# Kernel optimization log

Hardware: AMD Instinct MI355X
Metric: run time of the kernel (lower is better)

The kernel has to match this reference:

```python
import jax, jax.numpy as jnp
import numpy as np

B, D, C = 256, 128, 8000
MARGIN = 0.5
SCALE = 64.0
EPS = 1e-12  # tf.nn.l2_normalize epsilon


def _l2_normalize(x, axis):
    # Matches tf.nn.l2_normalize: x * rsqrt(max(sum(x^2), eps))
    sq = jnp.sum(x * x, axis=axis, keepdims=True)
    return x * jax.lax.rsqrt(jnp.maximum(sq, EPS))


def setup_inputs() -> dict:
    key = jax.random.key(0)
    k1, k2, k3 = jax.random.split(key, 3)
    embds = jax.random.normal(k1, (B, D), dtype=jnp.float32)
    w = jax.random.normal(k2, (D, C), dtype=jnp.float32)
    labels = jax.random.randint(k3, (B,), 0, C, dtype=jnp.int32)
    return {"embds": embds, "w": w, "labels": labels}


def reference(embds, w, labels):
    normed_embds = _l2_normalize(embds, axis=1)          # [B, D]
    normed_w = _l2_normalize(w, axis=0)                  # [D, C]
    gr_w = normed_w.T[labels]                            # gather per-label columns -> [B, D]
    # dw[b, d, c] = gr_w[b, d] - normed_w[d, c]
    dw = gr_w[:, :, None] - normed_w[None, :, :]         # [B, D, C]
    normed_dw = _l2_normalize(dw, axis=1)                # normalize over feature dim D
    win = jnp.einsum('bd,bdc->bc', normed_embds, normed_dw)
    penalties = MARGIN - jnp.minimum(MARGIN, win)        # [B, C]
    cos_t = normed_embds @ normed_w                      # [B, C]
    logits = jax.nn.softmax(SCALE * cos_t, axis=-1)
    return (logits, penalties)
```

## Files before the change

kernel.cpp:

```cpp
#include <hip/hip_runtime.h>
#include <math.h>

#define BB 256
#define DD 128
#define CC 8000
#define EPSF 1e-12f
#define SCALEF 64.0f
#define MARGINF 0.5f

__global__ __launch_bounds__(256, 2) void fused_kernel(
    const float* __restrict__ embds, const float* __restrict__ w,
    const int* __restrict__ labels, float* __restrict__ out,
    float* __restrict__ psums) {
  __shared__ float neS[DD * 16];
  __shared__ float gS[DD * 16];
  __shared__ float s1S[16];
  __shared__ int labS[16];

  int tid = threadIdx.x;
  int c0 = blockIdx.x * 256;
  int r0 = blockIdx.y * 16;

  {
    int r = tid >> 4;
    int k = tid & 15;
    int row = r0 + r;
    int lab = labels[row];
    const float4* e4 = (const float4*)(embds + row * DD + k * 8);
    float4 ea = e4[0], eb = e4[1];
    float ev[8] = {ea.x, ea.y, ea.z, ea.w, eb.x, eb.y, eb.z, eb.w};
    float wl[8];
    float se = 0.f, sw = 0.f, sx = 0.f;
    #pragma unroll
    for (int i = 0; i < 8; ++i) {
      wl[i] = w[(k * 8 + i) * CC + lab];
      se = fmaf(ev[i], ev[i], se);
      sw = fmaf(wl[i], wl[i], sw);
      sx = fmaf(ev[i], wl[i], sx);
    }
    #pragma unroll
    for (int off = 1; off < 16; off <<= 1) {
      se += __shfl_xor(se, off, 64);
      sw += __shfl_xor(sw, off, 64);
      sx += __shfl_xor(sx, off, 64);
    }
    float rn = rsqrtf(fmaxf(se, EPSF));
    float rl = rsqrtf(fmaxf(sw, EPSF));
    #pragma unroll
    for (int i = 0; i < 8; ++i) {
      neS[(k * 8 + i) * 16 + r] = ev[i] * rn;
      gS[(k * 8 + i) * 16 + r] = wl[i] * rl;
    }
    if (k == 0) { s1S[r] = sx * rn * rl; labS[r] = lab; }
  }
  __syncthreads();

  int tx = tid & 63;
  int ty = tid >> 6;
  int c = c0 + tx * 4;
  bool cok = c < CC;
  const float4* w4 = (const float4*)w;
  int wbase = (c0 >> 2) + tx;

  float accC[4][4], accG[4][4], colsum[4];
  #pragma unroll
  for (int rr = 0; rr < 4; ++rr)
    #pragma unroll
    for (int j = 0; j < 4; ++j) { accC[rr][j] = 0.f; accG[rr][j] = 0.f; }
  #pragma unroll
  for (int j = 0; j < 4; ++j) colsum[j] = 0.f;

  #pragma unroll 8
  for (int d = 0; d < DD; ++d) {
    float4 wv = cok ? w4[d * (CC / 4) + wbase] : make_float4(0.f, 0.f, 0.f, 0.f);
    float4 a = *(const float4*)&neS[d * 16 + ty * 4];
    float4 g = *(const float4*)&gS[d * 16 + ty * 4];
    float av[4] = {a.x, a.y, a.z, a.w};
    float gv[4] = {g.x, g.y, g.z, g.w};
    float wj[4] = {wv.x, wv.y, wv.z, wv.w};
    #pragma unroll
    for (int j = 0; j < 4; ++j) colsum[j] = fmaf(wj[j], wj[j], colsum[j]);
    #pragma unroll
    for (int rr = 0; rr < 4; ++rr) {
      #pragma unroll
      for (int j = 0; j < 4; ++j) {
        accC[rr][j] = fmaf(av[rr], wj[j], accC[rr][j]);
        accG[rr][j] = fmaf(gv[rr], wj[j], accG[rr][j]);
      }
    }
  }

  float rcj[4];
  #pragma unroll
  for (int j = 0; j < 4; ++j) rcj[j] = rsqrtf(fmaxf(colsum[j], EPSF));

  float* pen_base = out + (size_t)BB * CC;
  #pragma unroll
  for (int rr = 0; rr < 4; ++rr) {
    int lr = ty * 4 + rr;
    int row = r0 + lr;
    float s1v = s1S[lr];
    int lab = labS[lr];
    float penv[4], eo[4];
    float psum = 0.f;
    #pragma unroll
    for (int j = 0; j < 4; ++j) {
      float cs = accC[rr][j] * rcj[j];
      float gw = accG[rr][j] * rcj[j];
      float win = (s1v - cs) * rsqrtf(fmaxf(2.f - 2.f * gw, EPSF));
      if (c + j == lab) win = 0.f;
      penv[j] = MARGINF - fminf(MARGINF, win);
      float e = cok ? __expf(SCALEF * cs) : 0.f;
      eo[j] = e;
      psum += e;
    }
    if (cok) {
      size_t o4 = (size_t)row * (CC / 4) + wbase;
      ((float4*)pen_base)[o4] = make_float4(penv[0], penv[1], penv[2], penv[3]);
      ((float4*)out)[o4] = make_float4(eo[0], eo[1], eo[2], eo[3]);
    }
    #pragma unroll
    for (int off = 1; off < 64; off <<= 1) psum += __shfl_xor(psum, off, 64);
    if (tx == 0) psums[row * 32 + blockIdx.x] = psum;
  }
}

__global__ __launch_bounds__(512) void scale_kernel(
    float* __restrict__ out, const float* __restrict__ psums) {
  __shared__ float invS;
  int r = blockIdx.x;
  int tid = threadIdx.x;
  if (tid < 64) {
    float p = (tid < 32) ? psums[r * 32 + tid] : 0.f;
    #pragma unroll
    for (int off = 1; off < 32; off <<= 1) p += __shfl_xor(p, off, 64);
    if (tid == 0) invS = 1.f / p;
  }
  __syncthreads();
  float inv = invS;
  float4* row = (float4*)out + (size_t)r * (CC / 4);
  #pragma unroll
  for (int k = 0; k < 4; ++k) {
    int i = tid + k * 512;
    if (i < CC / 4) {
      float4 v = row[i];
      row[i] = make_float4(v.x * inv, v.y * inv, v.z * inv, v.w * inv);
    }
  }
}

extern "C" void kernel_launch(void* const* d_in, const int* in_sizes, int n_in,
                              void* d_out, int out_size, void* d_ws, size_t ws_size,
                              hipStream_t stream) {
  const float* embds = (const float*)d_in[0];
  const float* w = (const float*)d_in[1];
  const int* labels = (const int*)d_in[2];
  float* out = (float*)d_out;
  float* psums = (float*)d_ws;

  dim3 gA(32, 16);
  fused_kernel<<<gA, 256, 0, stream>>>(embds, w, labels, out, psums);
  scale_kernel<<<256, 512, 0, stream>>>(out, psums);
}
```

Measured before the change: 93.81 us.

## Stage W tiles through double-buffered shared memory with register prefetch

Each block now loads W in 16-row tiles into a double-buffered shared-memory array. The next tile is prefetched into registers while the current one is computed, and the first tile's load overlaps the normalization prologue. Before, every thread read W float4s straight from global memory inside the d-loop. Launch bounds rise to 3 blocks per SM, and the change adds about 32KB of LDS per block plus a barrier per tile. Edge columns are clamped, so tail blocks load duplicate data rather than zeros.

```diff
diff --git a/kernel.cpp b/kernel.cpp
--- a/kernel.cpp
+++ b/kernel.cpp
@@ -8,18 +8,38 @@
 #define SCALEF 64.0f
 #define MARGINF 0.5f
 
-__global__ __launch_bounds__(256, 2) void fused_kernel(
+#define RT 16
+#define CT 256
+#define TD 16
+#define NT (DD / TD)
+
+__global__ __launch_bounds__(256, 3) void fused_kernel(
     const float* __restrict__ embds, const float* __restrict__ w,
     const int* __restrict__ labels, float* __restrict__ out,
     float* __restrict__ psums) {
-  __shared__ float neS[DD * 16];
-  __shared__ float gS[DD * 16];
-  __shared__ float s1S[16];
-  __shared__ int labS[16];
+  __shared__ float wS[2][TD][CT];
+  __shared__ float neS[DD * RT];
+  __shared__ float gS[DD * RT];
+  __shared__ float s1S[RT];
+  __shared__ int labS[RT];
 
   int tid = threadIdx.x;
-  int c0 = blockIdx.x * 256;
-  int r0 = blockIdx.y * 16;
+  int c0 = blockIdx.x * CT;
+  int r0 = blockIdx.y * RT;
+
+  int sr = tid >> 4;
+  int scb = (tid & 15) * 4;
+  int scg[4];
+  #pragma unroll
+  for (int i = 0; i < 4; ++i) {
+    int cgl = c0 + scb + i * 64;
+    scg[i] = cgl > CC - 4 ? CC - 4 : cgl;
+  }
+
+  float4 st[4];
+  #pragma unroll
+  for (int i = 0; i < 4; ++i)
+    st[i] = *(const float4*)(w + (size_t)sr * CC + scg[i]);
 
   {
     int r = tid >> 4;
@@ -53,48 +73,67 @@
     }
     if (k == 0) { s1S[r] = sx * rn * rl; labS[r] = lab; }
   }
+
+  #pragma unroll
+  for (int i = 0; i < 4; ++i) *(float4*)&wS[0][sr][scb + i * 64] = st[i];
   __syncthreads();
 
   int tx = tid & 63;
   int ty = tid >> 6;
-  int c = c0 + tx * 4;
+  int wcol = tx * 4;
+  int c = c0 + wcol;
   bool cok = c < CC;
-  const float4* w4 = (const float4*)w;
+
+  float accC[4][4], accG[4][4], colsum[4];
+  #pragma unroll
+  for (int rr = 0; rr < 4; ++rr)
+    #pragma unroll
+    for (int j = 0; j < 4; ++j) { accC[rr][j] = 0.f; accG[rr][j] = 0.f; }
+  #pragma unroll
+  for (int j = 0; j < 4; ++j) colsum[j] = 0.f;
+
+  for (int t = 0; t < NT; ++t) {
+    if (t + 1 < NT) {
+      #pragma unroll
+      for (int i = 0; i < 4; ++i)
+        st[i] = *(const float4*)(w + (size_t)((t + 1) * TD + sr) * CC + scg[i]);
+    }
+
+    const float(*wT)[CT] = wS[t & 1];
+    #pragma unroll
+    for (int dl = 0; dl < TD; ++dl) {
+      int d = t * TD + dl;
+      float4 wv = *(const float4*)&wT[dl][wcol];
+      float4 a = *(const float4*)&neS[d * 16 + ty * 4];
+      float4 g = *(const float4*)&gS[d * 16 + ty * 4];
+      float av[4] = {a.x, a.y, a.z, a.w};
+      float gv[4] = {g.x, g.y, g.z, g.w};
+      float wj[4] = {wv.x, wv.y, wv.z, wv.w};
+      #pragma unroll
+      for (int j = 0; j < 4; ++j) colsum[j] = fmaf(wj[j], wj[j], colsum[j]);
+      #pragma unroll
+      for (int rr = 0; rr < 4; ++rr)
+        #pragma unroll
+        for (int j = 0; j < 4; ++j) {
+          accC[rr][j] = fmaf(av[rr], wj[j], accC[rr][j]);
+          accG[rr][j] = fmaf(gv[rr], wj[j], accG[rr][j]);
+        }
+    }
+
+    if (t + 1 < NT) {
+      #pragma unroll
+      for (int i = 0; i < 4; ++i)
+        *(float4*)&wS[(t + 1) & 1][sr][scb + i * 64] = st[i];
+    }
+    __syncthreads();
+  }
+
+  float rcj[4];
+  #pragma unroll
+  for (int j = 0; j < 4; ++j) rcj[j] = rsqrtf(fmaxf(colsum[j], EPSF));
+
+  float* pen_base = out + (size_t)BB * CC;
   int wbase = (c0 >> 2) + tx;
-
-  float accC[4][4], accG[4][4], colsum[4];
-  #pragma unroll
-  for (int rr = 0; rr < 4; ++rr)
-    #pragma unroll
-    for (int j = 0; j < 4; ++j) { accC[rr][j] = 0.f; accG[rr][j] = 0.f; }
-  #pragma unroll
-  for (int j = 0; j < 4; ++j) colsum[j] = 0.f;
-
-  #pragma unroll 8
-  for (int d = 0; d < DD; ++d) {
-    float4 wv = cok ? w4[d * (CC / 4) + wbase] : make_float4(0.f, 0.f, 0.f, 0.f);
-    float4 a = *(const float4*)&neS[d * 16 + ty * 4];
-    float4 g = *(const float4*)&gS[d * 16 + ty * 4];
-    float av[4] = {a.x, a.y, a.z, a.w};
-    float gv[4] = {g.x, g.y, g.z, g.w};
-    float wj[4] = {wv.x, wv.y, wv.z, wv.w};
-    #pragma unroll
-    for (int j = 0; j < 4; ++j) colsum[j] = fmaf(wj[j], wj[j], colsum[j]);
-    #pragma unroll
-    for (int rr = 0; rr < 4; ++rr) {
-      #pragma unroll
-      for (int j = 0; j < 4; ++j) {
-        accC[rr][j] = fmaf(av[rr], wj[j], accC[rr][j]);
-        accG[rr][j] = fmaf(gv[rr], wj[j], accG[rr][j]);
-      }
-    }
-  }
-
-  float rcj[4];
-  #pragma unroll
-  for (int j = 0; j < 4; ++j) rcj[j] = rsqrtf(fmaxf(colsum[j], EPSF));
-
-  float* pen_base = out + (size_t)BB * CC;
   #pragma unroll
   for (int rr = 0; rr < 4; ++rr) {
     int lr = ty * 4 + rr;
```

Result: slower. 197.3 us (+110.3%).

## Fuse softmax normalization into main kernel via last-block-per-row atomic ticket

Applied to the files above, without the earlier changes.

Removes the separate scale kernel launch. Each block publishes its partial exp-sum per row and increments a per-row atomic counter. The block that arrives last for a row reduces the partial sums and rescales that whole row in place. This saves a kernel launch and its gap, but the last-arriving blocks now do serial row rescaling work. The counter is never reset and relies on modulo 32 to work across repeated calls. Visibility of the other blocks' plain stores to the exp outputs rests only on the acq_rel ticket.

```diff
diff --git a/kernel.cpp b/kernel.cpp
--- a/kernel.cpp
+++ b/kernel.cpp
@@ -8,6 +8,9 @@
 #define SCALEF 64.0f
 #define MARGINF 0.5f
 
+
+__device__ int g_tick[BB];
+
 __global__ __launch_bounds__(256, 2) void fused_kernel(
     const float* __restrict__ embds, const float* __restrict__ w,
     const int* __restrict__ labels, float* __restrict__ out,
@@ -16,10 +19,14 @@
   __shared__ float gS[DD * 16];
   __shared__ float s1S[16];
   __shared__ int labS[16];
+  __shared__ int wonS[16];
+  __shared__ float invS;
 
   int tid = threadIdx.x;
   int c0 = blockIdx.x * 256;
   int r0 = blockIdx.y * 16;
+
+  if (tid < 16) wonS[tid] = 0;
 
   {
     int r = tid >> 4;
@@ -121,31 +128,36 @@
     }
     #pragma unroll
     for (int off = 1; off < 64; off <<= 1) psum += __shfl_xor(psum, off, 64);
-    if (tx == 0) psums[row * 32 + blockIdx.x] = psum;
-  }
-}
-
-__global__ __launch_bounds__(512) void scale_kernel(
-    float* __restrict__ out, const float* __restrict__ psums) {
-  __shared__ float invS;
-  int r = blockIdx.x;
-  int tid = threadIdx.x;
-  if (tid < 64) {
-    float p = (tid < 32) ? psums[r * 32 + tid] : 0.f;
-    #pragma unroll
-    for (int off = 1; off < 32; off <<= 1) p += __shfl_xor(p, off, 64);
-    if (tid == 0) invS = 1.f / p;
+    if (tx == 0) {
+      __hip_atomic_store(&psums[row * 32 + blockIdx.x], psum,
+                         __ATOMIC_RELAXED, __HIP_MEMORY_SCOPE_AGENT);
+      int old = __hip_atomic_fetch_add(&g_tick[row], 1, __ATOMIC_ACQ_REL,
+                                       __HIP_MEMORY_SCOPE_AGENT);
+      if ((old & 31) == 31) wonS[lr] = 1;
+    }
   }
   __syncthreads();
-  float inv = invS;
-  float4* row = (float4*)out + (size_t)r * (CC / 4);
-  #pragma unroll
-  for (int k = 0; k < 4; ++k) {
-    int i = tid + k * 512;
-    if (i < CC / 4) {
-      float4 v = row[i];
-      row[i] = make_float4(v.x * inv, v.y * inv, v.z * inv, v.w * inv);
+
+  for (int lr = 0; lr < 16; ++lr) {
+    if (!wonS[lr]) continue;
+    int row = r0 + lr;
+    if (tid < 64) {
+      float p = (tid < 32)
+                    ? __hip_atomic_load(&psums[row * 32 + tid], __ATOMIC_RELAXED,
+                                        __HIP_MEMORY_SCOPE_AGENT)
+                    : 0.f;
+      #pragma unroll
+      for (int off = 1; off < 32; off <<= 1) p += __shfl_xor(p, off, 64);
+      if (tid == 0) invS = 1.f / p;
     }
+    __syncthreads();
+    float inv = invS;
+    float4* rowp = (float4*)out + (size_t)row * (CC / 4);
+    for (int i = tid; i < CC / 4; i += 256) {
+      float4 v = rowp[i];
+      rowp[i] = make_float4(v.x * inv, v.y * inv, v.z * inv, v.w * inv);
+    }
+    __syncthreads();
   }
 }
 
@@ -160,5 +172,4 @@
 
   dim3 gA(32, 16);
   fused_kernel<<<gA, 256, 0, stream>>>(embds, w, labels, out, psums);
-  scale_kernel<<<256, 512, 0, stream>>>(out, psums);
 }
```

New measurement: 311.0 us. 3.32x slower.
